# Performance work log

Measured on AMD Instinct MI355X. Metric: run time of the kernel, lower is better.

Reference implementation:

```python
import jax, jax.numpy as jnp
import numpy as np

NUM_CLASSES = 19
MIN_SAMPLES = 1000.0
LOSS_WEIGHT = 1.0
TWO_PI = 2.0 * np.pi


def _nearest_upsample(x, H, W):
    # x: [D, h, w] -> [D, H, W]; matches torch F.interpolate(mode='nearest')
    h, w = x.shape[1], x.shape[2]
    ih = jnp.arange(H) * h // H
    iw = jnp.arange(W) * w // W
    return x[:, ih][:, :, iw]


def _smooth_l1(a, b):
    # F.smooth_l1_loss with beta=1.0, mean reduction
    d = jnp.abs(a - b)
    return jnp.mean(jnp.where(d < 1.0, 0.5 * d * d, d - 0.5))


def setup_inputs() -> dict:
    key = jax.random.key(0)
    k1, k2 = jax.random.split(key)
    feature = jax.random.normal(k1, (1, 64, 128, 128), dtype=jnp.float32)
    label = jax.random.randint(k2, (1, 1, 512, 512), 0, NUM_CLASSES)
    return {"feature": feature, "label": label}


def reference(feature, label):
    D = feature.shape[1]
    H, W = label.shape[2], label.shape[3]
    feat = _nearest_upsample(feature[0], H, W).reshape(D, -1)   # [D, P]
    lab = label[0, 0].reshape(-1)                               # [P]
    ks = jnp.arange(-3, 4, dtype=feat.dtype)                    # 7 gaussian bins

    def per_class(c):
        mask = (lab == c).astype(feat.dtype)                    # [P]
        n = jnp.sum(mask)
        n_safe = jnp.maximum(n, 1.0)
        miu = (feat * mask).sum(1) / n_safe                     # [D]
        var = (((feat - miu[:, None]) ** 2) * mask).sum(1) / n_safe + 1e-10
        std = jnp.sqrt(var)
        var_s = var / 25.0
        bins = miu[:, None] + ks[None, :] * std[:, None]        # [D, 7]
        # KDE: sum over class pixels of N(bin; feat_p, var_s), vectorized over bins
        z2 = (bins[:, :, None] - feat[:, None, :]) ** 2 / var_s[:, None, None]  # [D,7,P]
        sample_values = (jnp.exp(-0.5 * z2) * mask[None, None, :]).sum(-1) / jnp.sqrt(TWO_PI * var_s)[:, None]
        # target computed under no_grad in the original: bin - miu = k*std
        target_values = jax.lax.stop_gradient(
            jnp.exp(-0.5 * ks ** 2)[None, :] / jnp.sqrt(TWO_PI * var)[:, None]
        )
        hist = sample_values / jnp.maximum(sample_values.sum(1, keepdims=True), 1e-30)
        targ = target_values / target_values.sum(1, keepdims=True)
        active = (n >= MIN_SAMPLES).astype(feat.dtype)
        return _smooth_l1(hist, targ) * active, active

    losses, actives = jax.lax.map(per_class, jnp.arange(NUM_CLASSES))
    return LOSS_WEIGHT * jnp.sum(losses) / jnp.sum(actives)
```

## Files before the change

kernel.cpp:

```cpp
#include <hip/hip_runtime.h>
#include <hip/hip_bf16.h>

#define SRC   16384
#define DCH   64
#define NCLS  19
#define NPAIR (NCLS*DCH)
#define KSPLIT 2

#if defined(__has_builtin)
#if __has_builtin(__builtin_amdgcn_exp2f)
#define EXP2F(x) __builtin_amdgcn_exp2f(x)
#else
#define EXP2F(x) __builtin_exp2f(x)
#endif
#else
#define EXP2F(x) __builtin_exp2f(x)
#endif

__global__ __launch_bounds__(256) void hl_count_kernel(
    const int* __restrict__ label, unsigned char* __restrict__ cnt)
{
    int s  = blockIdx.x * 256 + threadIdx.x;
    int sy = s >> 7, sx = s & 127;
    const int4* lab4 = (const int4*)label;
    int l[16];
#pragma unroll
    for (int r = 0; r < 4; r++) {
        int4 v = lab4[(4 * sy + r) * 128 + sx];
        l[4 * r + 0] = v.x; l[4 * r + 1] = v.y;
        l[4 * r + 2] = v.z; l[4 * r + 3] = v.w;
    }
#pragma unroll
    for (int c = 0; c < NCLS; c++) {
        int cc = 0;
#pragma unroll
        for (int j = 0; j < 16; j++) cc += (l[j] == c) ? 1 : 0;
        cnt[c * SRC + s] = (unsigned char)cc;
    }
}

__global__ __launch_bounds__(1024) void hl_moments_kernel(
    const float* __restrict__ feature, const unsigned char* __restrict__ cnt,
    double* __restrict__ S1, double* __restrict__ S2, int* __restrict__ ncls)
{
    int w = blockIdx.x;
    int c = w >> 6, d = w & 63;
    int tid = threadIdx.x;

    const float4*       fp4 = (const float4*)(feature + d * SRC);
    const unsigned int* cp4 = (const unsigned int*)(cnt + c * SRC);

    float f1 = 0.f, f2 = 0.f;
    int   nc = 0;
#pragma unroll
    for (int i = 0; i < 4; i++) {
        int g = i * 1024 + tid;
        float4       x  = fp4[g];
        unsigned int cv = cp4[g];
        float xs[4] = {x.x, x.y, x.z, x.w};
        float cf[4] = {(float)(cv & 255u), (float)((cv >> 8) & 255u),
                       (float)((cv >> 16) & 255u), (float)(cv >> 24)};
#pragma unroll
        for (int e = 0; e < 4; e++) {
            float wx = cf[e] * xs[e];
            f1 += wx;
            f2 = fmaf(wx, xs[e], f2);
        }
        nc += (cv & 255u) + ((cv >> 8) & 255u) + ((cv >> 16) & 255u) + (cv >> 24);
    }
    double s1 = (double)f1, s2 = (double)f2;
#pragma unroll
    for (int o = 32; o > 0; o >>= 1) {
        s1 += __shfl_down(s1, o);
        s2 += __shfl_down(s2, o);
        nc += __shfl_down(nc, o);
    }
    __shared__ double ps1[16], ps2[16];
    __shared__ int    pn[16];
    int wid = tid >> 6;
    if ((tid & 63) == 0) { ps1[wid] = s1; ps2[wid] = s2; pn[wid] = nc; }
    __syncthreads();
    if (tid == 0) {
        double a = 0.0, b = 0.0; int n = 0;
#pragma unroll
        for (int i = 0; i < 16; i++) { a += ps1[i]; b += ps2[i]; n += pn[i]; }
        S1[w] = a; S2[w] = b;
        if (d == 0) ncls[c] = n;
    }
}

__global__ __launch_bounds__(1024) void hl_kde_kernel(
    const float* __restrict__ feature, const unsigned char* __restrict__ cnt,
    const double* __restrict__ S1d, const double* __restrict__ S2d,
    const int* __restrict__ ncls, float* __restrict__ sample)
{
    int blk  = blockIdx.x;
    int w    = blk >> 1;
    int half = blk & 1;
    int c = w >> 6, d = w & 63;
    int tid = threadIdx.x;

    __shared__ float sh_mu, sh_istd;
    if (tid == 0) {
        int    n     = ncls[c];
        double nsafe = (n > 0) ? (double)n : 1.0;
        double s1 = S1d[w], s2 = S2d[w];
        double mu  = s1 / nsafe;
        double var = (s2 - 2.0 * mu * s1 + mu * mu * (double)n) / nsafe + 1e-10;
        sh_mu   = (float)mu;
        sh_istd = (float)(1.0 / sqrt(var));
    }
    __syncthreads();
    float istd = sh_istd;
    float nm   = -sh_mu * istd;

    const float4*       fp4 = (const float4*)(feature + d * SRC);
    const unsigned int* cp4 = (const unsigned int*)(cnt + c * SRC);

    const float C1 = -18.033688011112042f;
    float acc[7] = {0.f, 0.f, 0.f, 0.f, 0.f, 0.f, 0.f};

#pragma unroll
    for (int i = 0; i < 2; i++) {
        int g = half * 2048 + i * 1024 + tid;
        float4       x  = fp4[g];
        unsigned int cv = cp4[g];
        float xs[4] = {x.x, x.y, x.z, x.w};
        float cf[4] = {(float)(cv & 255u), (float)((cv >> 8) & 255u),
                       (float)((cv >> 16) & 255u), (float)(cv >> 24)};
#pragma unroll
        for (int e = 0; e < 4; e++) {
            float u = fmaf(xs[e], istd, nm);
            float p = C1 * u;
            float q = p * u;
#pragma unroll
            for (int k = 0; k < 7; k++) {
                float km = (float)(k - 3);
                float arg = fmaf(p, -2.f * km, q + C1 * km * km);
                acc[k] = fmaf(cf[e], EXP2F(arg), acc[k]);
            }
        }
    }

    __shared__ float part[16][7];
    int wid = tid >> 6;
#pragma unroll
    for (int j = 0; j < 7; j++) {
        float v = acc[j];
#pragma unroll
        for (int o = 32; o > 0; o >>= 1) v += __shfl_down(v, o);
        if ((tid & 63) == 0) part[wid][j] = v;
    }
    __syncthreads();
    if (tid < 7) {
        float v = 0.f;
#pragma unroll
        for (int i = 0; i < 16; i++) v += part[i][tid];
        sample[blk * 7 + tid] = v;
    }
}

__global__ __launch_bounds__(512) void hl_loss_kernel(
    const float* __restrict__ sample, const int* __restrict__ ncls,
    float* __restrict__ out)
{
    int tid = threadIdx.x;

    float targ[7];
    {
        double e[7], z = 0.0;
#pragma unroll
        for (int k = -3; k <= 3; k++) { e[k + 3] = exp(-0.5 * (double)(k * k)); z += e[k + 3]; }
#pragma unroll
        for (int j = 0; j < 7; j++) targ[j] = (float)(e[j] / z);
    }

    float lsum = 0.f, asum = 0.f;
    for (int p = tid; p < NPAIR; p += 512) {
        int c = p >> 6;
        int n = ncls[c];
        if (n < 1000) continue;
        float sv[7], S = 0.f;
#pragma unroll
        for (int j = 0; j < 7; j++) {
            sv[j] = sample[(2 * p) * 7 + j] + sample[(2 * p + 1) * 7 + j];
            S += sv[j];
        }
        float Ss = fmaxf(S, 1e-30f);
        float ps = 0.f;
#pragma unroll
        for (int j = 0; j < 7; j++) {
            float dd = fabsf(sv[j] / Ss - targ[j]);
            ps += (dd < 1.f) ? 0.5f * dd * dd : (dd - 0.5f);
        }
        lsum += ps;
        if ((p & 63) == 0) asum += 1.f;
    }

#pragma unroll
    for (int o = 32; o > 0; o >>= 1) {
        lsum += __shfl_down(lsum, o);
        asum += __shfl_down(asum, o);
    }
    __shared__ float lw[8], aw[8];
    int wid = tid >> 6;
    if ((tid & 63) == 0) { lw[wid] = lsum; aw[wid] = asum; }
    __syncthreads();
    if (tid == 0) {
        float L = 0.f, A = 0.f;
#pragma unroll
        for (int i = 0; i < 8; i++) { L += lw[i]; A += aw[i]; }
        out[0] = (A > 0.f) ? (L / 448.0f) / A : 0.0f;
    }
}

extern "C" void kernel_launch(void* const* d_in, const int* in_sizes, int n_in,
                              void* d_out, int out_size, void* d_ws, size_t ws_size,
                              hipStream_t stream)
{
    const float* feature = (const float*)d_in[0];
    const int*   label   = (const int*)d_in[1];
    float*       out     = (float*)d_out;

    char* ws = (char*)d_ws;
    unsigned char* cnt    = (unsigned char*)(ws);
    double*        S1     = (double*)(ws + 311296);
    double*        S2     = (double*)(ws + 311296 + 9728);
    int*           ncls   = (int*)(ws + 311296 + 2 * 9728);
    float*         sample = (float*)(ws + 311296 + 2 * 9728 + 128);

    hl_count_kernel<<<SRC / 256, 256, 0, stream>>>(label, cnt);
    hl_moments_kernel<<<NPAIR, 1024, 0, stream>>>(feature, cnt, S1, S2, ncls);
    hl_kde_kernel<<<NPAIR * KSPLIT, 1024, 0, stream>>>(feature, cnt, S1, S2, ncls, sample);
    hl_loss_kernel<<<1, 512, 0, stream>>>(sample, ncls, out);
}
```

Before: 96.70 us.

## Fuse four kernels into one persistent kernel with grid-wide barriers

Replaces the count, moments, KDE and loss kernels with a single persistent kernel of 512 blocks that loops over work items and separates the phases with atomic-counter grid barriers, plus a tiny init kernel that resets the counter. This removes three kernel launch boundaries and their tail and drain gaps. In exchange it depends on all 512 blocks of 1024 threads being co-resident, otherwise the spin barrier deadlocks. Each phase also runs with fewer blocks than before, looping instead of launching one block per item.

```diff
diff --git a/kernel.cpp b/kernel.cpp
--- a/kernel.cpp
+++ b/kernel.cpp
@@ -5,7 +5,8 @@
 #define DCH   64
 #define NCLS  19
 #define NPAIR (NCLS*DCH)
-#define KSPLIT 2
+#define NBLK  512
+#define NITEM (NPAIR*2)
 
 #if defined(__has_builtin)
 #if __has_builtin(__builtin_amdgcn_exp2f)
@@ -17,154 +18,169 @@
 #define EXP2F(x) __builtin_exp2f(x)
 #endif
 
-__global__ __launch_bounds__(256) void hl_count_kernel(
-    const int* __restrict__ label, unsigned char* __restrict__ cnt)
-{
-    int s  = blockIdx.x * 256 + threadIdx.x;
-    int sy = s >> 7, sx = s & 127;
-    const int4* lab4 = (const int4*)label;
-    int l[16];
-#pragma unroll
-    for (int r = 0; r < 4; r++) {
-        int4 v = lab4[(4 * sy + r) * 128 + sx];
-        l[4 * r + 0] = v.x; l[4 * r + 1] = v.y;
-        l[4 * r + 2] = v.z; l[4 * r + 3] = v.w;
-    }
-#pragma unroll
-    for (int c = 0; c < NCLS; c++) {
-        int cc = 0;
-#pragma unroll
-        for (int j = 0; j < 16; j++) cc += (l[j] == c) ? 1 : 0;
-        cnt[c * SRC + s] = (unsigned char)cc;
-    }
-}
-
-__global__ __launch_bounds__(1024) void hl_moments_kernel(
-    const float* __restrict__ feature, const unsigned char* __restrict__ cnt,
-    double* __restrict__ S1, double* __restrict__ S2, int* __restrict__ ncls)
-{
-    int w = blockIdx.x;
-    int c = w >> 6, d = w & 63;
-    int tid = threadIdx.x;
-
-    const float4*       fp4 = (const float4*)(feature + d * SRC);
-    const unsigned int* cp4 = (const unsigned int*)(cnt + c * SRC);
-
-    float f1 = 0.f, f2 = 0.f;
-    int   nc = 0;
-#pragma unroll
-    for (int i = 0; i < 4; i++) {
-        int g = i * 1024 + tid;
-        float4       x  = fp4[g];
-        unsigned int cv = cp4[g];
-        float xs[4] = {x.x, x.y, x.z, x.w};
-        float cf[4] = {(float)(cv & 255u), (float)((cv >> 8) & 255u),
-                       (float)((cv >> 16) & 255u), (float)(cv >> 24)};
-#pragma unroll
-        for (int e = 0; e < 4; e++) {
-            float wx = cf[e] * xs[e];
-            f1 += wx;
-            f2 = fmaf(wx, xs[e], f2);
-        }
-        nc += (cv & 255u) + ((cv >> 8) & 255u) + ((cv >> 16) & 255u) + (cv >> 24);
-    }
-    double s1 = (double)f1, s2 = (double)f2;
-#pragma unroll
-    for (int o = 32; o > 0; o >>= 1) {
-        s1 += __shfl_down(s1, o);
-        s2 += __shfl_down(s2, o);
-        nc += __shfl_down(nc, o);
-    }
+__global__ void hl_init_kernel(unsigned* __restrict__ bar)
+{
+    __hip_atomic_store(bar, 0u, __ATOMIC_RELAXED, __HIP_MEMORY_SCOPE_SYSTEM);
+}
+
+__device__ __forceinline__ void grid_barrier(unsigned* bar, unsigned target)
+{
+    __syncthreads();
+    if (threadIdx.x == 0) {
+        __threadfence();
+        __hip_atomic_fetch_add(bar, 1u, __ATOMIC_RELAXED, __HIP_MEMORY_SCOPE_AGENT);
+        while (__hip_atomic_load(bar, __ATOMIC_RELAXED, __HIP_MEMORY_SCOPE_AGENT) < target)
+            __builtin_amdgcn_s_sleep(2);
+        __threadfence();
+    }
+    __syncthreads();
+}
+
+__global__ __launch_bounds__(1024, 8) void hl_fused_kernel(
+    const float* __restrict__ feature, const int* __restrict__ label,
+    unsigned char* __restrict__ cnt,
+    double* __restrict__ S1, double* __restrict__ S2, int* __restrict__ ncls,
+    float* __restrict__ sample, unsigned* __restrict__ bar,
+    float* __restrict__ out)
+{
+    const int tid = threadIdx.x;
+    const int wid = tid >> 6;
+
     __shared__ double ps1[16], ps2[16];
     __shared__ int    pn[16];
-    int wid = tid >> 6;
-    if ((tid & 63) == 0) { ps1[wid] = s1; ps2[wid] = s2; pn[wid] = nc; }
-    __syncthreads();
-    if (tid == 0) {
-        double a = 0.0, b = 0.0; int n = 0;
-#pragma unroll
-        for (int i = 0; i < 16; i++) { a += ps1[i]; b += ps2[i]; n += pn[i]; }
-        S1[w] = a; S2[w] = b;
-        if (d == 0) ncls[c] = n;
-    }
-}
-
-__global__ __launch_bounds__(1024) void hl_kde_kernel(
-    const float* __restrict__ feature, const unsigned char* __restrict__ cnt,
-    const double* __restrict__ S1d, const double* __restrict__ S2d,
-    const int* __restrict__ ncls, float* __restrict__ sample)
-{
-    int blk  = blockIdx.x;
-    int w    = blk >> 1;
-    int half = blk & 1;
-    int c = w >> 6, d = w & 63;
-    int tid = threadIdx.x;
-
-    __shared__ float sh_mu, sh_istd;
-    if (tid == 0) {
-        int    n     = ncls[c];
-        double nsafe = (n > 0) ? (double)n : 1.0;
-        double s1 = S1d[w], s2 = S2d[w];
-        double mu  = s1 / nsafe;
-        double var = (s2 - 2.0 * mu * s1 + mu * mu * (double)n) / nsafe + 1e-10;
-        sh_mu   = (float)mu;
-        sh_istd = (float)(1.0 / sqrt(var));
-    }
-    __syncthreads();
-    float istd = sh_istd;
-    float nm   = -sh_mu * istd;
-
-    const float4*       fp4 = (const float4*)(feature + d * SRC);
-    const unsigned int* cp4 = (const unsigned int*)(cnt + c * SRC);
-
-    const float C1 = -18.033688011112042f;
-    float acc[7] = {0.f, 0.f, 0.f, 0.f, 0.f, 0.f, 0.f};
-
-#pragma unroll
-    for (int i = 0; i < 2; i++) {
-        int g = half * 2048 + i * 1024 + tid;
-        float4       x  = fp4[g];
-        unsigned int cv = cp4[g];
-        float xs[4] = {x.x, x.y, x.z, x.w};
-        float cf[4] = {(float)(cv & 255u), (float)((cv >> 8) & 255u),
-                       (float)((cv >> 16) & 255u), (float)(cv >> 24)};
-#pragma unroll
-        for (int e = 0; e < 4; e++) {
-            float u = fmaf(xs[e], istd, nm);
-            float p = C1 * u;
-            float q = p * u;
-#pragma unroll
-            for (int k = 0; k < 7; k++) {
-                float km = (float)(k - 3);
-                float arg = fmaf(p, -2.f * km, q + C1 * km * km);
-                acc[k] = fmaf(cf[e], EXP2F(arg), acc[k]);
+    __shared__ float  part[16][7];
+    __shared__ float  sh_mu, sh_istd;
+    __shared__ float  lw[16], aw[16];
+
+    if (blockIdx.x < 16) {
+        int s  = blockIdx.x * 1024 + tid;
+        int sy = s >> 7, sx = s & 127;
+        const int4* lab4 = (const int4*)label;
+        int l[16];
+#pragma unroll
+        for (int r = 0; r < 4; r++) {
+            int4 v = lab4[(4 * sy + r) * 128 + sx];
+            l[4 * r + 0] = v.x; l[4 * r + 1] = v.y;
+            l[4 * r + 2] = v.z; l[4 * r + 3] = v.w;
+        }
+#pragma unroll
+        for (int c = 0; c < NCLS; c++) {
+            int cc = 0;
+#pragma unroll
+            for (int j = 0; j < 16; j++) cc += (l[j] == c) ? 1 : 0;
+            cnt[c * SRC + s] = (unsigned char)cc;
+        }
+    }
+    grid_barrier(bar, NBLK);
+
+    for (int w = blockIdx.x; w < NPAIR; w += NBLK) {
+        int c = w >> 6, d = w & 63;
+        const float4*       fp4 = (const float4*)(feature + d * SRC);
+        const unsigned int* cp4 = (const unsigned int*)(cnt + c * SRC);
+
+        float f1 = 0.f, f2 = 0.f;
+        int   nc = 0;
+#pragma unroll
+        for (int i = 0; i < 4; i++) {
+            int g = i * 1024 + tid;
+            float4       x  = fp4[g];
+            unsigned int cv = cp4[g];
+            float xs[4] = {x.x, x.y, x.z, x.w};
+            float cf[4] = {(float)(cv & 255u), (float)((cv >> 8) & 255u),
+                           (float)((cv >> 16) & 255u), (float)(cv >> 24)};
+#pragma unroll
+            for (int e = 0; e < 4; e++) {
+                float wx = cf[e] * xs[e];
+                f1 += wx;
+                f2 = fmaf(wx, xs[e], f2);
             }
-        }
-    }
-
-    __shared__ float part[16][7];
-    int wid = tid >> 6;
-#pragma unroll
-    for (int j = 0; j < 7; j++) {
-        float v = acc[j];
-#pragma unroll
-        for (int o = 32; o > 0; o >>= 1) v += __shfl_down(v, o);
-        if ((tid & 63) == 0) part[wid][j] = v;
-    }
-    __syncthreads();
-    if (tid < 7) {
-        float v = 0.f;
-#pragma unroll
-        for (int i = 0; i < 16; i++) v += part[i][tid];
-        sample[blk * 7 + tid] = v;
-    }
-}
-
-__global__ __launch_bounds__(512) void hl_loss_kernel(
-    const float* __restrict__ sample, const int* __restrict__ ncls,
-    float* __restrict__ out)
-{
-    int tid = threadIdx.x;
+            nc += (cv & 255u) + ((cv >> 8) & 255u) + ((cv >> 16) & 255u) + (cv >> 24);
+        }
+        double s1 = (double)f1, s2 = (double)f2;
+#pragma unroll
+        for (int o = 32; o > 0; o >>= 1) {
+            s1 += __shfl_down(s1, o);
+            s2 += __shfl_down(s2, o);
+            nc += __shfl_down(nc, o);
+        }
+        if ((tid & 63) == 0) { ps1[wid] = s1; ps2[wid] = s2; pn[wid] = nc; }
+        __syncthreads();
+        if (tid == 0) {
+            double a = 0.0, b = 0.0; int n = 0;
+#pragma unroll
+            for (int i = 0; i < 16; i++) { a += ps1[i]; b += ps2[i]; n += pn[i]; }
+            S1[w] = a; S2[w] = b;
+            if (d == 0) ncls[c] = n;
+        }
+        __syncthreads();
+    }
+    grid_barrier(bar, 2 * NBLK);
+
+    for (int item = blockIdx.x; item < NITEM; item += NBLK) {
+        int w    = item >> 1;
+        int half = item & 1;
+        int c = w >> 6, d = w & 63;
+
+        if (tid == 0) {
+            int    n     = ncls[c];
+            double nsafe = (n > 0) ? (double)n : 1.0;
+            double s1 = S1[w], s2 = S2[w];
+            double mu  = s1 / nsafe;
+            double var = (s2 - 2.0 * mu * s1 + mu * mu * (double)n) / nsafe + 1e-10;
+            sh_mu   = (float)mu;
+            sh_istd = (float)(1.0 / sqrt(var));
+        }
+        __syncthreads();
+        float istd = sh_istd;
+        float nm   = -sh_mu * istd;
+
+        const float4*       fp4 = (const float4*)(feature + d * SRC);
+        const unsigned int* cp4 = (const unsigned int*)(cnt + c * SRC);
+
+        const float C1 = -18.033688011112042f;
+        float acc[7] = {0.f, 0.f, 0.f, 0.f, 0.f, 0.f, 0.f};
+
+#pragma unroll
+        for (int i = 0; i < 2; i++) {
+            int g = half * 2048 + i * 1024 + tid;
+            float4       x  = fp4[g];
+            unsigned int cv = cp4[g];
+            float xs[4] = {x.x, x.y, x.z, x.w};
+            float cf[4] = {(float)(cv & 255u), (float)((cv >> 8) & 255u),
+                           (float)((cv >> 16) & 255u), (float)(cv >> 24)};
+#pragma unroll
+            for (int e = 0; e < 4; e++) {
+                float u = fmaf(xs[e], istd, nm);
+                float p = C1 * u;
+                float q = p * u;
+#pragma unroll
+                for (int k = 0; k < 7; k++) {
+                    float km  = (float)(k - 3);
+                    float arg = fmaf(p, -2.f * km, q + C1 * km * km);
+                    acc[k] = fmaf(cf[e], EXP2F(arg), acc[k]);
+                }
+            }
+        }
+
+#pragma unroll
+        for (int j = 0; j < 7; j++) {
+            float v = acc[j];
+#pragma unroll
+            for (int o = 32; o > 0; o >>= 1) v += __shfl_down(v, o);
+            if ((tid & 63) == 0) part[wid][j] = v;
+        }
+        __syncthreads();
+        if (tid < 7) {
+            float v = 0.f;
+#pragma unroll
+            for (int i = 0; i < 16; i++) v += part[i][tid];
+            sample[item * 7 + tid] = v;
+        }
+        __syncthreads();
+    }
+    grid_barrier(bar, 3 * NBLK);
+
+    if (blockIdx.x != 0) return;
 
     float targ[7];
     {
@@ -176,7 +192,7 @@
     }
 
     float lsum = 0.f, asum = 0.f;
-    for (int p = tid; p < NPAIR; p += 512) {
+    for (int p = tid; p < NPAIR; p += 1024) {
         int c = p >> 6;
         int n = ncls[c];
         if (n < 1000) continue;
@@ -196,20 +212,17 @@
         lsum += ps;
         if ((p & 63) == 0) asum += 1.f;
     }
-
 #pragma unroll
     for (int o = 32; o > 0; o >>= 1) {
         lsum += __shfl_down(lsum, o);
         asum += __shfl_down(asum, o);
     }
-    __shared__ float lw[8], aw[8];
-    int wid = tid >> 6;
     if ((tid & 63) == 0) { lw[wid] = lsum; aw[wid] = asum; }
     __syncthreads();
     if (tid == 0) {
         float L = 0.f, A = 0.f;
 #pragma unroll
-        for (int i = 0; i < 8; i++) { L += lw[i]; A += aw[i]; }
+        for (int i = 0; i < 16; i++) { L += lw[i]; A += aw[i]; }
         out[0] = (A > 0.f) ? (L / 448.0f) / A : 0.0f;
     }
 }
@@ -228,9 +241,9 @@
     double*        S2     = (double*)(ws + 311296 + 9728);
     int*           ncls   = (int*)(ws + 311296 + 2 * 9728);
     float*         sample = (float*)(ws + 311296 + 2 * 9728 + 128);
-
-    hl_count_kernel<<<SRC / 256, 256, 0, stream>>>(label, cnt);
-    hl_moments_kernel<<<NPAIR, 1024, 0, stream>>>(feature, cnt, S1, S2, ncls);
-    hl_kde_kernel<<<NPAIR * KSPLIT, 1024, 0, stream>>>(feature, cnt, S1, S2, ncls, sample);
-    hl_loss_kernel<<<1, 512, 0, stream>>>(sample, ncls, out);
-}
+    unsigned*      bar    = (unsigned*)(ws + 399104);
+
+    hl_init_kernel<<<1, 1, 0, stream>>>(bar);
+    hl_fused_kernel<<<NBLK, 1024, 0, stream>>>(feature, label, cnt, S1, S2, ncls,
+                                               sample, bar, out);
+}
```

After: 211.7 us. 2.19x slower.

## Split moment reduction into chunked partial-sum stage and per-class final reduction

Applied to the files above, without the earlier changes.

The per-(class,channel) moments kernel, which re-read the feature and count arrays once per pair (1216 blocks), becomes two stages. Stage A reads each pixel chunk once for all 19 classes and writes float partial sums per chunk. Stage B reduces those partials in double per class. This cuts redundant global reads of the feature map but adds a kernel launch, a partial buffer of about 2.5 MB, and float rather than double accumulation inside each chunk.

```diff
diff --git a/kernel.cpp b/kernel.cpp
--- a/kernel.cpp
+++ b/kernel.cpp
@@ -1,20 +1,22 @@
 #include <hip/hip_runtime.h>
 #include <hip/hip_bf16.h>
 
-#define SRC   16384
-#define DCH   64
-#define NCLS  19
-#define NPAIR (NCLS*DCH)
+#define SRC    16384
+#define DCH    64
+#define NCLS   19
+#define NPAIR  (NCLS*DCH)
+#define NCHUNK 256
+#define CPX    64
 #define KSPLIT 2
 
 #if defined(__has_builtin)
 #if __has_builtin(__builtin_amdgcn_exp2f)
 #define EXP2F(x) __builtin_amdgcn_exp2f(x)
 #else
-#define EXP2F(x) __builtin_exp2f(x)
+#define EXP2F(x) __exp2f(x)
 #endif
 #else
-#define EXP2F(x) __builtin_exp2f(x)
+#define EXP2F(x) __exp2f(x)
 #endif
 
 __global__ __launch_bounds__(256) void hl_count_kernel(
@@ -39,54 +41,108 @@
     }
 }
 
-__global__ __launch_bounds__(1024) void hl_moments_kernel(
+__global__ __launch_bounds__(256) void hl_stageA_kernel(
     const float* __restrict__ feature, const unsigned char* __restrict__ cnt,
+    float* __restrict__ P1, float* __restrict__ P2, int* __restrict__ PN)
+{
+    int cb = blockIdx.x;
+    int t  = threadIdx.x;
+    int d  = t & 63, g = t >> 6;
+    int s0 = cb * CPX;
+
+    const float4* f4 = (const float4*)(feature + d * SRC + s0 + 16 * g);
+    float xs[16];
+#pragma unroll
+    for (int i = 0; i < 4; i++) {
+        float4 v = f4[i];
+        xs[4 * i + 0] = v.x; xs[4 * i + 1] = v.y;
+        xs[4 * i + 2] = v.z; xs[4 * i + 3] = v.w;
+    }
+
+    float a1[NCLS], a2[NCLS];
+#pragma unroll
+    for (int c = 0; c < NCLS; c++) {
+        const uint4* c4 = (const uint4*)(cnt + c * SRC + s0 + 16 * g);
+        uint4 cw = *c4;
+        unsigned int wdw[4] = {cw.x, cw.y, cw.z, cw.w};
+        float s1 = 0.f, s2 = 0.f;
+#pragma unroll
+        for (int q = 0; q < 4; q++) {
+#pragma unroll
+            for (int b = 0; b < 4; b++) {
+                float cv = (float)((wdw[q] >> (8 * b)) & 0xFFu);
+                float x  = xs[4 * q + b];
+                float wx = cv * x;
+                s1 += wx;
+                s2 = fmaf(wx, x, s2);
+            }
+        }
+        a1[c] = s1; a2[c] = s2;
+    }
+
+    __shared__ float b1[NPAIR], b2[NPAIR];
+#pragma unroll
+    for (int r = 0; r < 4; r++) {
+        if (g == r) {
+            if (r == 0) {
+#pragma unroll
+                for (int c = 0; c < NCLS; c++) { b1[c * 64 + d] = a1[c]; b2[c * 64 + d] = a2[c]; }
+            } else {
+#pragma unroll
+                for (int c = 0; c < NCLS; c++) { b1[c * 64 + d] += a1[c]; b2[c * 64 + d] += a2[c]; }
+            }
+        }
+        __syncthreads();
+    }
+    for (int i = t; i < NPAIR; i += 256) {
+        P1[cb * NPAIR + i] = b1[i];
+        P2[cb * NPAIR + i] = b2[i];
+    }
+    if (t < NCLS) {
+        const uint4* cr = (const uint4*)(cnt + t * SRC + s0);
+        int n = 0;
+#pragma unroll
+        for (int i = 0; i < 4; i++) {
+            uint4 v = cr[i];
+            unsigned int ww[4] = {v.x, v.y, v.z, v.w};
+#pragma unroll
+            for (int q = 0; q < 4; q++)
+                n += (ww[q] & 0xFF) + ((ww[q] >> 8) & 0xFF) + ((ww[q] >> 16) & 0xFF) + (ww[q] >> 24);
+        }
+        PN[cb * NCLS + t] = n;
+    }
+}
+
+__global__ __launch_bounds__(1024) void hl_stageB_kernel(
+    const float* __restrict__ P1, const float* __restrict__ P2,
+    const int* __restrict__ PN,
     double* __restrict__ S1, double* __restrict__ S2, int* __restrict__ ncls)
 {
-    int w = blockIdx.x;
-    int c = w >> 6, d = w & 63;
-    int tid = threadIdx.x;
-
-    const float4*       fp4 = (const float4*)(feature + d * SRC);
-    const unsigned int* cp4 = (const unsigned int*)(cnt + c * SRC);
-
-    float f1 = 0.f, f2 = 0.f;
-    int   nc = 0;
-#pragma unroll
-    for (int i = 0; i < 4; i++) {
-        int g = i * 1024 + tid;
-        float4       x  = fp4[g];
-        unsigned int cv = cp4[g];
-        float xs[4] = {x.x, x.y, x.z, x.w};
-        float cf[4] = {(float)(cv & 255u), (float)((cv >> 8) & 255u),
-                       (float)((cv >> 16) & 255u), (float)(cv >> 24)};
-#pragma unroll
-        for (int e = 0; e < 4; e++) {
-            float wx = cf[e] * xs[e];
-            f1 += wx;
-            f2 = fmaf(wx, xs[e], f2);
-        }
-        nc += (cv & 255u) + ((cv >> 8) & 255u) + ((cv >> 16) & 255u) + (cv >> 24);
-    }
-    double s1 = (double)f1, s2 = (double)f2;
-#pragma unroll
-    for (int o = 32; o > 0; o >>= 1) {
+    int c = blockIdx.x;
+    int t = threadIdx.x;
+    int d = t >> 4, j = t & 15;
+
+    double s1 = 0.0, s2 = 0.0;
+    for (int ch = j; ch < NCHUNK; ch += 16) {
+        s1 += (double)P1[ch * NPAIR + c * 64 + d];
+        s2 += (double)P2[ch * NPAIR + c * 64 + d];
+    }
+#pragma unroll
+    for (int o = 8; o > 0; o >>= 1) {
         s1 += __shfl_down(s1, o);
         s2 += __shfl_down(s2, o);
-        nc += __shfl_down(nc, o);
-    }
-    __shared__ double ps1[16], ps2[16];
-    __shared__ int    pn[16];
-    int wid = tid >> 6;
-    if ((tid & 63) == 0) { ps1[wid] = s1; ps2[wid] = s2; pn[wid] = nc; }
-    __syncthreads();
-    if (tid == 0) {
-        double a = 0.0, b = 0.0; int n = 0;
-#pragma unroll
-        for (int i = 0; i < 16; i++) { a += ps1[i]; b += ps2[i]; n += pn[i]; }
-        S1[w] = a; S2[w] = b;
-        if (d == 0) ncls[c] = n;
-    }
+    }
+    if (j == 0) { S1[c * 64 + d] = s1; S2[c * 64 + d] = s2; }
+
+    __shared__ int nb[4];
+    if (t < NCHUNK) {
+        int n = PN[t * NCLS + c];
+#pragma unroll
+        for (int o = 32; o > 0; o >>= 1) n += __shfl_down(n, o);
+        if ((t & 63) == 0) nb[t >> 6] = n;
+    }
+    __syncthreads();
+    if (t == 0) ncls[c] = nb[0] + nb[1] + nb[2] + nb[3];
 }
 
 __global__ __launch_bounds__(1024) void hl_kde_kernel(
@@ -135,7 +191,7 @@
             float q = p * u;
 #pragma unroll
             for (int k = 0; k < 7; k++) {
-                float km = (float)(k - 3);
+                float km  = (float)(k - 3);
                 float arg = fmaf(p, -2.f * km, q + C1 * km * km);
                 acc[k] = fmaf(cf[e], EXP2F(arg), acc[k]);
             }
@@ -196,7 +252,6 @@
         lsum += ps;
         if ((p & 63) == 0) asum += 1.f;
     }
-
 #pragma unroll
     for (int o = 32; o > 0; o >>= 1) {
         lsum += __shfl_down(lsum, o);
@@ -224,13 +279,17 @@
 
     char* ws = (char*)d_ws;
     unsigned char* cnt    = (unsigned char*)(ws);
-    double*        S1     = (double*)(ws + 311296);
-    double*        S2     = (double*)(ws + 311296 + 9728);
-    int*           ncls   = (int*)(ws + 311296 + 2 * 9728);
-    float*         sample = (float*)(ws + 311296 + 2 * 9728 + 128);
-
-    hl_count_kernel<<<SRC / 256, 256, 0, stream>>>(label, cnt);
-    hl_moments_kernel<<<NPAIR, 1024, 0, stream>>>(feature, cnt, S1, S2, ncls);
-    hl_kde_kernel<<<NPAIR * KSPLIT, 1024, 0, stream>>>(feature, cnt, S1, S2, ncls, sample);
-    hl_loss_kernel<<<1, 512, 0, stream>>>(sample, ncls, out);
-}
+    float*         P1     = (float*)(ws + 311296);
+    float*         P2     = (float*)(ws + 1556480);
+    int*           PN     = (int*)(ws + 2801664);
+    double*        S1     = (double*)(ws + 2821120);
+    double*        S2     = (double*)(ws + 2830848);
+    int*           ncls   = (int*)(ws + 2840576);
+    float*         sample = (float*)(ws + 2840704);
+
+    hl_count_kernel <<<SRC / 256, 256, 0, stream>>>(label, cnt);
+    hl_stageA_kernel<<<NCHUNK, 256, 0, stream>>>(feature, cnt, P1, P2, PN);
+    hl_stageB_kernel<<<NCLS, 1024, 0, stream>>>(P1, P2, PN, S1, S2, ncls);
+    hl_kde_kernel   <<<NPAIR * KSPLIT, 1024, 0, stream>>>(feature, cnt, S1, S2, ncls, sample);
+    hl_loss_kernel  <<<1, 512, 0, stream>>>(sample, ncls, out);
+}
```

Result: slower. 110.6 us (+14.3%).

## Fuse loss reduction into KDE kernel with atomics and skip inactive classes

Applied to the files above, without the earlier changes.

Removes the final single-block loss kernel. Each KDE block now computes its own smooth-L1 contribution and atomically adds it to the output, which is zeroed in the count kernel. KDE and moments blocks shrink from 1024 to 256 threads, each thread covering all 16 iterations, and the KSPLIT split is dropped. KDE blocks for classes below the sample threshold return early. This saves one launch and a buffer round trip, at the cost of a non-deterministic float atomic summation order and fewer threads per block.

```diff
diff --git a/kernel.cpp b/kernel.cpp
--- a/kernel.cpp
+++ b/kernel.cpp
@@ -1,25 +1,26 @@
 #include <hip/hip_runtime.h>
 #include <hip/hip_bf16.h>
 
-#define SRC   16384
-#define DCH   64
-#define NCLS  19
-#define NPAIR (NCLS*DCH)
-#define KSPLIT 2
+#define SRC    16384
+#define DCH    64
+#define NCLS   19
+#define NPAIR  (NCLS*DCH)
 
 #if defined(__has_builtin)
 #if __has_builtin(__builtin_amdgcn_exp2f)
 #define EXP2F(x) __builtin_amdgcn_exp2f(x)
 #else
-#define EXP2F(x) __builtin_exp2f(x)
+#define EXP2F(x) __exp2f(x)
 #endif
 #else
-#define EXP2F(x) __builtin_exp2f(x)
+#define EXP2F(x) __exp2f(x)
 #endif
 
 __global__ __launch_bounds__(256) void hl_count_kernel(
-    const int* __restrict__ label, unsigned char* __restrict__ cnt)
-{
+    const int* __restrict__ label, unsigned char* __restrict__ cnt,
+    float* __restrict__ out)
+{
+    if (blockIdx.x == 0 && threadIdx.x == 0) out[0] = 0.f;
     int s  = blockIdx.x * 256 + threadIdx.x;
     int sy = s >> 7, sx = s & 127;
     const int4* lab4 = (const int4*)label;
@@ -39,24 +40,24 @@
     }
 }
 
-__global__ __launch_bounds__(1024) void hl_moments_kernel(
+__global__ __launch_bounds__(256) void hl_moments_kernel(
     const float* __restrict__ feature, const unsigned char* __restrict__ cnt,
     double* __restrict__ S1, double* __restrict__ S2, int* __restrict__ ncls)
 {
     int w = blockIdx.x;
     int c = w >> 6, d = w & 63;
-    int tid = threadIdx.x;
+    int t = threadIdx.x;
 
     const float4*       fp4 = (const float4*)(feature + d * SRC);
-    const unsigned int* cp4 = (const unsigned int*)(cnt + c * SRC);
+    const unsigned int* cpu = (const unsigned int*)(cnt + c * SRC);
 
     float f1 = 0.f, f2 = 0.f;
     int   nc = 0;
 #pragma unroll
-    for (int i = 0; i < 4; i++) {
-        int g = i * 1024 + tid;
+    for (int i = 0; i < 16; i++) {
+        int g = i * 256 + t;
         float4       x  = fp4[g];
-        unsigned int cv = cp4[g];
+        unsigned int cv = cpu[g];
         float xs[4] = {x.x, x.y, x.z, x.w};
         float cf[4] = {(float)(cv & 255u), (float)((cv >> 8) & 255u),
                        (float)((cv >> 16) & 255u), (float)(cv >> 24)};
@@ -75,33 +76,33 @@
         s2 += __shfl_down(s2, o);
         nc += __shfl_down(nc, o);
     }
-    __shared__ double ps1[16], ps2[16];
-    __shared__ int    pn[16];
-    int wid = tid >> 6;
-    if ((tid & 63) == 0) { ps1[wid] = s1; ps2[wid] = s2; pn[wid] = nc; }
+    __shared__ double ps1[4], ps2[4];
+    __shared__ int    pn[4];
+    int wid = t >> 6;
+    if ((t & 63) == 0) { ps1[wid] = s1; ps2[wid] = s2; pn[wid] = nc; }
     __syncthreads();
-    if (tid == 0) {
-        double a = 0.0, b = 0.0; int n = 0;
-#pragma unroll
-        for (int i = 0; i < 16; i++) { a += ps1[i]; b += ps2[i]; n += pn[i]; }
+    if (t == 0) {
+        double a = ps1[0] + ps1[1] + ps1[2] + ps1[3];
+        double b = ps2[0] + ps2[1] + ps2[2] + ps2[3];
+        int    n = pn[0] + pn[1] + pn[2] + pn[3];
         S1[w] = a; S2[w] = b;
         if (d == 0) ncls[c] = n;
     }
 }
 
-__global__ __launch_bounds__(1024) void hl_kde_kernel(
+__global__ __launch_bounds__(256) void hl_kde_kernel(
     const float* __restrict__ feature, const unsigned char* __restrict__ cnt,
     const double* __restrict__ S1d, const double* __restrict__ S2d,
-    const int* __restrict__ ncls, float* __restrict__ sample)
-{
-    int blk  = blockIdx.x;
-    int w    = blk >> 1;
-    int half = blk & 1;
+    const int* __restrict__ ncls, float* __restrict__ out)
+{
+    int w = blockIdx.x;
     int c = w >> 6, d = w & 63;
-    int tid = threadIdx.x;
+    int t = threadIdx.x;
+    int wid = t >> 6;
 
     __shared__ float sh_mu, sh_istd;
-    if (tid == 0) {
+    __shared__ int   sh_act;
+    if (t == 0) {
         int    n     = ncls[c];
         double nsafe = (n > 0) ? (double)n : 1.0;
         double s1 = S1d[w], s2 = S2d[w];
@@ -109,22 +110,24 @@
         double var = (s2 - 2.0 * mu * s1 + mu * mu * (double)n) / nsafe + 1e-10;
         sh_mu   = (float)mu;
         sh_istd = (float)(1.0 / sqrt(var));
+        sh_act  = (n >= 1000);
     }
     __syncthreads();
+    if (!sh_act) return;
     float istd = sh_istd;
     float nm   = -sh_mu * istd;
 
     const float4*       fp4 = (const float4*)(feature + d * SRC);
-    const unsigned int* cp4 = (const unsigned int*)(cnt + c * SRC);
+    const unsigned int* cpu = (const unsigned int*)(cnt + c * SRC);
 
     const float C1 = -18.033688011112042f;
     float acc[7] = {0.f, 0.f, 0.f, 0.f, 0.f, 0.f, 0.f};
 
 #pragma unroll
-    for (int i = 0; i < 2; i++) {
-        int g = half * 2048 + i * 1024 + tid;
+    for (int i = 0; i < 16; i++) {
+        int g = i * 256 + t;
         float4       x  = fp4[g];
-        unsigned int cv = cp4[g];
+        unsigned int cv = cpu[g];
         float xs[4] = {x.x, x.y, x.z, x.w};
         float cf[4] = {(float)(cv & 255u), (float)((cv >> 8) & 255u),
                        (float)((cv >> 16) & 255u), (float)(cv >> 24)};
@@ -135,82 +138,45 @@
             float q = p * u;
 #pragma unroll
             for (int k = 0; k < 7; k++) {
-                float km = (float)(k - 3);
+                float km  = (float)(k - 3);
                 float arg = fmaf(p, -2.f * km, q + C1 * km * km);
                 acc[k] = fmaf(cf[e], EXP2F(arg), acc[k]);
             }
         }
     }
 
-    __shared__ float part[16][7];
-    int wid = tid >> 6;
+    __shared__ float part[4][7];
 #pragma unroll
     for (int j = 0; j < 7; j++) {
         float v = acc[j];
 #pragma unroll
         for (int o = 32; o > 0; o >>= 1) v += __shfl_down(v, o);
-        if ((tid & 63) == 0) part[wid][j] = v;
+        if ((t & 63) == 0) part[wid][j] = v;
     }
     __syncthreads();
-    if (tid < 7) {
-        float v = 0.f;
-#pragma unroll
-        for (int i = 0; i < 16; i++) v += part[i][tid];
-        sample[blk * 7 + tid] = v;
-    }
-}
-
-__global__ __launch_bounds__(512) void hl_loss_kernel(
-    const float* __restrict__ sample, const int* __restrict__ ncls,
-    float* __restrict__ out)
-{
-    int tid = threadIdx.x;
-
-    float targ[7];
-    {
+
+    if (t == 0) {
         double e[7], z = 0.0;
 #pragma unroll
         for (int k = -3; k <= 3; k++) { e[k + 3] = exp(-0.5 * (double)(k * k)); z += e[k + 3]; }
-#pragma unroll
-        for (int j = 0; j < 7; j++) targ[j] = (float)(e[j] / z);
-    }
-
-    float lsum = 0.f, asum = 0.f;
-    for (int p = tid; p < NPAIR; p += 512) {
-        int c = p >> 6;
-        int n = ncls[c];
-        if (n < 1000) continue;
-        float sv[7], S = 0.f;
+
+        float hist[7], S = 0.f;
 #pragma unroll
         for (int j = 0; j < 7; j++) {
-            sv[j] = sample[(2 * p) * 7 + j] + sample[(2 * p + 1) * 7 + j];
-            S += sv[j];
+            hist[j] = part[0][j] + part[1][j] + part[2][j] + part[3][j];
+            S += hist[j];
         }
         float Ss = fmaxf(S, 1e-30f);
         float ps = 0.f;
 #pragma unroll
         for (int j = 0; j < 7; j++) {
-            float dd = fabsf(sv[j] / Ss - targ[j]);
+            float dd = fabsf(hist[j] / Ss - (float)(e[j] / z));
             ps += (dd < 1.f) ? 0.5f * dd * dd : (dd - 0.5f);
         }
-        lsum += ps;
-        if ((p & 63) == 0) asum += 1.f;
-    }
-
-#pragma unroll
-    for (int o = 32; o > 0; o >>= 1) {
-        lsum += __shfl_down(lsum, o);
-        asum += __shfl_down(asum, o);
-    }
-    __shared__ float lw[8], aw[8];
-    int wid = tid >> 6;
-    if ((tid & 63) == 0) { lw[wid] = lsum; aw[wid] = asum; }
-    __syncthreads();
-    if (tid == 0) {
-        float L = 0.f, A = 0.f;
-#pragma unroll
-        for (int i = 0; i < 8; i++) { L += lw[i]; A += aw[i]; }
-        out[0] = (A > 0.f) ? (L / 448.0f) / A : 0.0f;
+        int A = 0;
+#pragma unroll
+        for (int i = 0; i < NCLS; i++) A += (ncls[i] >= 1000) ? 1 : 0;
+        atomicAdd(out, ps / (448.0f * (float)A));
     }
 }
 
@@ -223,14 +189,12 @@
     float*       out     = (float*)d_out;
 
     char* ws = (char*)d_ws;
-    unsigned char* cnt    = (unsigned char*)(ws);
-    double*        S1     = (double*)(ws + 311296);
-    double*        S2     = (double*)(ws + 311296 + 9728);
-    int*           ncls   = (int*)(ws + 311296 + 2 * 9728);
-    float*         sample = (float*)(ws + 311296 + 2 * 9728 + 128);
-
-    hl_count_kernel<<<SRC / 256, 256, 0, stream>>>(label, cnt);
-    hl_moments_kernel<<<NPAIR, 1024, 0, stream>>>(feature, cnt, S1, S2, ncls);
-    hl_kde_kernel<<<NPAIR * KSPLIT, 1024, 0, stream>>>(feature, cnt, S1, S2, ncls, sample);
-    hl_loss_kernel<<<1, 512, 0, stream>>>(sample, ncls, out);
-}
+    unsigned char* cnt  = (unsigned char*)(ws);
+    double*        S1   = (double*)(ws + 311296);
+    double*        S2   = (double*)(ws + 321024);
+    int*           ncls = (int*)(ws + 330752);
+
+    hl_count_kernel  <<<SRC / 256, 256, 0, stream>>>(label, cnt, out);
+    hl_moments_kernel<<<NPAIR, 256, 0, stream>>>(feature, cnt, S1, S2, ncls);
+    hl_kde_kernel    <<<NPAIR, 256, 0, stream>>>(feature, cnt, S1, S2, ncls, out);
+}
```

Result: slower. 117.9 us (+21.9%).
